# Kernel optimization log

Hardware: AMD Instinct MI355X
Metric: run time of the kernel (lower is better)

## Reference

```python
import jax, jax.numpy as jnp
import numpy as np

S = 30.0  # scale
M = 0.5   # angular margin

N, D, C = 1024, 512, 100000


def setup_inputs() -> dict:
    key = jax.random.key(0)
    k1, k2, k3 = jax.random.split(key, 3)
    embeddings = jax.random.normal(k1, (N, D), dtype=jnp.float32)
    weight = jax.random.normal(k2, (C, D), dtype=jnp.float32)
    labels = jax.random.randint(k3, (N,), 0, C, dtype=jnp.int64)
    return {"embeddings": embeddings, "weight": weight, "labels": labels}


def _l2norm(x, axis=-1, eps=1e-12):
    # matches torch F.normalize: x / max(||x||, eps)
    n = jnp.sqrt(jnp.sum(x * x, axis=axis, keepdims=True))
    return x / jnp.maximum(n, eps)


def reference(embeddings, weight, labels):
    e = _l2norm(embeddings)                      # [N, D]
    w = _l2norm(weight)                          # [C, D]
    cos_theta = jnp.clip(e @ w.T, -1.0, 1.0)     # [N, C]
    theta = jnp.arccos(cos_theta)
    cos_theta_m = jnp.cos(theta + M)
    # apply margin only at the label-indexed entry per row (one-hot blend)
    rows = jnp.arange(cos_theta.shape[0])
    target_vals = cos_theta_m[rows, labels]
    logits = cos_theta.at[rows, labels].set(target_vals)
    return S * logits
```

## Files before the change

### kernel.cpp

```cpp
#include <hip/hip_runtime.h>
#include <cstdint>
#include <cstddef>


constexpr int N_ROWS = 1024;
constexpr int DIM    = 512;
constexpr int C_CLS  = 100000;
constexpr int C_PAD  = 100096;

#define COS_M 0.87758256189037271612f
#define SIN_M 0.47942553860420300027f

typedef __attribute__((ext_vector_type(8))) __bf16 bf16x8;
typedef __attribute__((ext_vector_type(4))) float  floatx4;

__device__ inline unsigned short f2bf(float f) {
    unsigned int u = __float_as_uint(f);
    u += 0x7FFFu + ((u >> 16) & 1u);
    return (unsigned short)(u >> 16);
}

__device__ inline float wave_reduce_sum(float v) {
    v += __shfl_xor(v, 32, 64);
    v += __shfl_xor(v, 16, 64);
    v += __shfl_xor(v, 8, 64);
    v += __shfl_xor(v, 4, 64);
    v += __shfl_xor(v, 2, 64);
    v += __shfl_xor(v, 1, 64);
    return v;
}

__device__ inline void async16(const void* g, void* l) {
    __builtin_amdgcn_global_load_lds(
        (const __attribute__((address_space(1))) void*)g,
        (__attribute__((address_space(3))) void*)l,
        16, 0, 0);
}

__global__ __launch_bounds__(256) void normalize_rows(
    const float* __restrict__ in, unsigned short* __restrict__ out,
    int rows_valid, int rows_total) {
    int wave = (int)((blockIdx.x * 256u + threadIdx.x) >> 6);
    int lane = threadIdx.x & 63;
    if (wave >= rows_total) return;

    unsigned short* orow = out + (size_t)wave * DIM;
    if (wave < rows_valid) {
        const float4* rp = (const float4*)(in + (size_t)wave * DIM);
        float4 x0 = rp[lane];
        float4 x1 = rp[64 + lane];
        float s = x0.x*x0.x + x0.y*x0.y + x0.z*x0.z + x0.w*x0.w
                + x1.x*x1.x + x1.y*x1.y + x1.z*x1.z + x1.w*x1.w;
        s = wave_reduce_sum(s);
        float inv = 1.0f / fmaxf(sqrtf(s), 1e-12f);
        ushort4 o0, o1;
        o0.x = f2bf(x0.x * inv); o0.y = f2bf(x0.y * inv);
        o0.z = f2bf(x0.z * inv); o0.w = f2bf(x0.w * inv);
        o1.x = f2bf(x1.x * inv); o1.y = f2bf(x1.y * inv);
        o1.z = f2bf(x1.z * inv); o1.w = f2bf(x1.w * inv);
        ((ushort4*)orow)[lane]      = o0;
        ((ushort4*)orow)[64 + lane] = o1;
    } else {
        ushort4 z; z.x = z.y = z.z = z.w = 0;
        ((ushort4*)orow)[lane]      = z;
        ((ushort4*)orow)[64 + lane] = z;
    }
}

__global__ __launch_bounds__(256) void arcface_gemm(
    const unsigned short* __restrict__ A,
    const unsigned short* __restrict__ W,
    const int* __restrict__ labels,
    float* __restrict__ out) {
    __shared__ unsigned short As[128 * 32];
    __shared__ unsigned short Bs[128 * 32];
    __shared__ int labs[128];

    const int tid  = threadIdx.x;
    const int lane = tid & 63;
    const int wv   = tid >> 6;
    const int wr   = wv >> 1;
    const int wc   = wv & 1;
    const int mbase = blockIdx.x * 128;
    const int nbase = blockIdx.y * 128;

    if (tid < 128) labs[tid] = labels[mbase + tid];

    const int srow   = tid >> 2;
    const int schunk = tid & 3;

    floatx4 acc[4][4];
    for (int i = 0; i < 4; i++)
        for (int j = 0; j < 4; j++)
            acc[i][j] = (floatx4){0.f, 0.f, 0.f, 0.f};

    const unsigned short* Ag = A + (size_t)mbase * DIM;
    const unsigned short* Wg = W + (size_t)nbase * DIM;

    const int kq   = (lane >> 4) * 8;
    const int mrow = lane & 15;

    for (int k0 = 0; k0 < DIM; k0 += 32) {
        async16(Ag + (size_t)srow * DIM + k0 + schunk * 8,        &As[tid * 8]);
        async16(Ag + (size_t)(srow + 64) * DIM + k0 + schunk * 8, &As[2048 + tid * 8]);
        async16(Wg + (size_t)srow * DIM + k0 + schunk * 8,        &Bs[tid * 8]);
        async16(Wg + (size_t)(srow + 64) * DIM + k0 + schunk * 8, &Bs[2048 + tid * 8]);
        __syncthreads();

        bf16x8 af[4], bfr[4];
        for (int i = 0; i < 4; i++)
            af[i] = *(const bf16x8*)&As[(wr * 64 + i * 16 + mrow) * 32 + kq];
        for (int j = 0; j < 4; j++)
            bfr[j] = *(const bf16x8*)&Bs[(wc * 64 + j * 16 + mrow) * 32 + kq];

        for (int i = 0; i < 4; i++)
            for (int j = 0; j < 4; j++)
                acc[i][j] = __builtin_amdgcn_mfma_f32_16x16x32_bf16(
                    af[i], bfr[j], acc[i][j], 0, 0, 0);
        __syncthreads();
    }

    const int col0 = nbase + wc * 64 + (lane & 15);
    for (int i = 0; i < 4; i++) {
        const int rbase = wr * 64 + i * 16 + (lane >> 4) * 4;
        for (int r = 0; r < 4; r++) {
            const int row  = rbase + r;
            const int grow = mbase + row;
            const int lab  = labs[row];
            float* orow = out + (size_t)grow * C_CLS;
            for (int j = 0; j < 4; j++) {
                const int gc = col0 + j * 16;
                if (gc < C_CLS) {
                    float c = acc[i][j][r];
                    c = fminf(1.0f, fmaxf(-1.0f, c));
                    float v = c;
                    if (gc == lab) {
                        v = COS_M * c - SIN_M * sqrtf(fmaxf(0.0f, 1.0f - c * c));
                    }
                    orow[gc] = 30.0f * v;
                }
            }
        }
    }
}

extern "C" void kernel_launch(void* const* d_in, const int* in_sizes, int n_in,
                              void* d_out, int out_size, void* d_ws, size_t ws_size,
                              hipStream_t stream) {
    const float* emb    = (const float*)d_in[0];
    const float* wgt    = (const float*)d_in[1];
    const int*   labels = (const int*)d_in[2];
    float*       out    = (float*)d_out;

    unsigned short* An = (unsigned short*)d_ws;
    unsigned short* Wn = (unsigned short*)((char*)d_ws + (size_t)N_ROWS * DIM * 2);

    normalize_rows<<<N_ROWS / 4, 256, 0, stream>>>(emb, An, N_ROWS, N_ROWS);
    normalize_rows<<<C_PAD / 4, 256, 0, stream>>>(wgt, Wn, C_CLS, C_PAD);

    dim3 grid(N_ROWS / 128, C_PAD / 128);
    arcface_gemm<<<grid, 256, 0, stream>>>(An, Wn, labels, out);
}
```

Before: 727.7 us.

## Fuse weight normalization into GEMM and remap blocks for XCD L2 reuse

Drops the separate weight-normalization kernel: the GEMM now loads fp32 weight rows directly, converts them to bf16 in registers, accumulates per-row sums of squares, and scales the accumulators by the inverse norm in the epilogue. Blocks are remapped so all M tiles of a weight panel land on the same XCD for L2 sharing, and LDS tiles use XOR swizzling to reduce bank conflicts. This removes a full read/write pass over the weight matrix, at the cost of twice the B-tile load bytes per K step and extra conversion work in the main loop.

```diff
diff --git a/kernel.cpp b/kernel.cpp
--- a/kernel.cpp
+++ b/kernel.cpp
@@ -6,7 +6,8 @@
 constexpr int N_ROWS = 1024;
 constexpr int DIM    = 512;
 constexpr int C_CLS  = 100000;
-constexpr int C_PAD  = 100096;
+constexpr int NPANEL = 784;
+constexpr int MTILES = 8;
 
 #define COS_M 0.87758256189037271612f
 #define SIN_M 0.47942553860420300027f
@@ -38,100 +39,165 @@
 }
 
 __global__ __launch_bounds__(256) void normalize_rows(
-    const float* __restrict__ in, unsigned short* __restrict__ out,
-    int rows_valid, int rows_total) {
+    const float* __restrict__ in, unsigned short* __restrict__ out, int rows) {
     int wave = (int)((blockIdx.x * 256u + threadIdx.x) >> 6);
     int lane = threadIdx.x & 63;
-    if (wave >= rows_total) return;
-
+    if (wave >= rows) return;
+
+    const float4* rp = (const float4*)(in + (size_t)wave * DIM);
+    float4 x0 = rp[lane];
+    float4 x1 = rp[64 + lane];
+    float s = x0.x*x0.x + x0.y*x0.y + x0.z*x0.z + x0.w*x0.w
+            + x1.x*x1.x + x1.y*x1.y + x1.z*x1.z + x1.w*x1.w;
+    s = wave_reduce_sum(s);
+    float inv = 1.0f / fmaxf(sqrtf(s), 1e-12f);
     unsigned short* orow = out + (size_t)wave * DIM;
-    if (wave < rows_valid) {
-        const float4* rp = (const float4*)(in + (size_t)wave * DIM);
-        float4 x0 = rp[lane];
-        float4 x1 = rp[64 + lane];
-        float s = x0.x*x0.x + x0.y*x0.y + x0.z*x0.z + x0.w*x0.w
-                + x1.x*x1.x + x1.y*x1.y + x1.z*x1.z + x1.w*x1.w;
-        s = wave_reduce_sum(s);
-        float inv = 1.0f / fmaxf(sqrtf(s), 1e-12f);
-        ushort4 o0, o1;
-        o0.x = f2bf(x0.x * inv); o0.y = f2bf(x0.y * inv);
-        o0.z = f2bf(x0.z * inv); o0.w = f2bf(x0.w * inv);
-        o1.x = f2bf(x1.x * inv); o1.y = f2bf(x1.y * inv);
-        o1.z = f2bf(x1.z * inv); o1.w = f2bf(x1.w * inv);
-        ((ushort4*)orow)[lane]      = o0;
-        ((ushort4*)orow)[64 + lane] = o1;
-    } else {
-        ushort4 z; z.x = z.y = z.z = z.w = 0;
-        ((ushort4*)orow)[lane]      = z;
-        ((ushort4*)orow)[64 + lane] = z;
-    }
+    ushort4 o0, o1;
+    o0.x = f2bf(x0.x * inv); o0.y = f2bf(x0.y * inv);
+    o0.z = f2bf(x0.z * inv); o0.w = f2bf(x0.w * inv);
+    o1.x = f2bf(x1.x * inv); o1.y = f2bf(x1.y * inv);
+    o1.z = f2bf(x1.z * inv); o1.w = f2bf(x1.w * inv);
+    ((ushort4*)orow)[lane]      = o0;
+    ((ushort4*)orow)[64 + lane] = o1;
 }
 
 __global__ __launch_bounds__(256) void arcface_gemm(
     const unsigned short* __restrict__ A,
-    const unsigned short* __restrict__ W,
+    const float* __restrict__ Wf,
     const int* __restrict__ labels,
     float* __restrict__ out) {
     __shared__ unsigned short As[128 * 32];
-    __shared__ unsigned short Bs[128 * 32];
-    __shared__ int labs[128];
+    __shared__ float          Bs[128 * 32];
+    __shared__ int   labs[128];
+    __shared__ float winv[128];
 
     const int tid  = threadIdx.x;
     const int lane = tid & 63;
     const int wv   = tid >> 6;
     const int wr   = wv >> 1;
     const int wc   = wv & 1;
-    const int mbase = blockIdx.x * 128;
-    const int nbase = blockIdx.y * 128;
+
+    const int bid   = blockIdx.x;
+    const int xcd   = bid & 7;
+    const int s     = bid >> 3;
+    const int panel = xcd * (NPANEL / 8) + (s >> 3);
+    const int mtile = s & 7;
+    const int mbase = mtile * 128;
+    const int nbase = panel * 128;
 
     if (tid < 128) labs[tid] = labels[mbase + tid];
 
-    const int srow   = tid >> 2;
-    const int schunk = tid & 3;
+    const int arow0  = tid >> 2;
+    const int aslot0 = (tid & 3) ^ (arow0 & 3);
+    const int arow1  = arow0 + 64;
+    const int aslot1 = (tid & 3) ^ (arow1 & 3);
+    size_t bsrc[4];
+    #pragma unroll
+    for (int q = 0; q < 4; q++) {
+        int c    = tid + 256 * q;
+        int row  = c >> 3;
+        int slot = (c & 7) ^ (row & 7);
+        int grow = nbase + row;
+        if (grow > C_CLS - 1) grow = C_CLS - 1;
+        bsrc[q] = (size_t)grow * DIM + (size_t)(slot * 4);
+    }
+
+    const unsigned short* Ag = A + (size_t)mbase * DIM;
+
+    const int kq   = (lane >> 4) * 8;
+    const int mrow = lane & 15;
+
+    int aidx[4];
+    #pragma unroll
+    for (int i = 0; i < 4; i++) {
+        int row = wr * 64 + i * 16 + mrow;
+        aidx[i] = row * 32 + (((kq >> 3) ^ (row & 3)) << 3);
+    }
+    int bidx0[4], bidx1[4];
+    #pragma unroll
+    for (int j = 0; j < 4; j++) {
+        int row  = wc * 64 + j * 16 + mrow;
+        bidx0[j] = row * 32 + ((((kq >> 2)    ) ^ (row & 7)) << 2);
+        bidx1[j] = row * 32 + ((((kq >> 2) + 1) ^ (row & 7)) << 2);
+    }
 
     floatx4 acc[4][4];
+    #pragma unroll
     for (int i = 0; i < 4; i++)
+        #pragma unroll
         for (int j = 0; j < 4; j++)
             acc[i][j] = (floatx4){0.f, 0.f, 0.f, 0.f};
-
-    const unsigned short* Ag = A + (size_t)mbase * DIM;
-    const unsigned short* Wg = W + (size_t)nbase * DIM;
-
-    const int kq   = (lane >> 4) * 8;
-    const int mrow = lane & 15;
+    float ssq[2] = {0.f, 0.f};
 
     for (int k0 = 0; k0 < DIM; k0 += 32) {
-        async16(Ag + (size_t)srow * DIM + k0 + schunk * 8,        &As[tid * 8]);
-        async16(Ag + (size_t)(srow + 64) * DIM + k0 + schunk * 8, &As[2048 + tid * 8]);
-        async16(Wg + (size_t)srow * DIM + k0 + schunk * 8,        &Bs[tid * 8]);
-        async16(Wg + (size_t)(srow + 64) * DIM + k0 + schunk * 8, &Bs[2048 + tid * 8]);
+        async16(Ag + (size_t)arow0 * DIM + k0 + aslot0 * 8, &As[tid * 8]);
+        async16(Ag + (size_t)arow1 * DIM + k0 + aslot1 * 8, &As[2048 + tid * 8]);
+        #pragma unroll
+        for (int q = 0; q < 4; q++)
+            async16(Wf + bsrc[q] + k0, &Bs[(tid + 256 * q) * 4]);
         __syncthreads();
 
         bf16x8 af[4], bfr[4];
+        #pragma unroll
         for (int i = 0; i < 4; i++)
-            af[i] = *(const bf16x8*)&As[(wr * 64 + i * 16 + mrow) * 32 + kq];
-        for (int j = 0; j < 4; j++)
-            bfr[j] = *(const bf16x8*)&Bs[(wc * 64 + j * 16 + mrow) * 32 + kq];
-
+            af[i] = *(const bf16x8*)&As[aidx[i]];
+        #pragma unroll
+        for (int j = 0; j < 4; j++) {
+            float4 lo = *(const float4*)&Bs[bidx0[j]];
+            float4 hi = *(const float4*)&Bs[bidx1[j]];
+            bf16x8 b;
+            b[0] = (__bf16)lo.x; b[1] = (__bf16)lo.y;
+            b[2] = (__bf16)lo.z; b[3] = (__bf16)lo.w;
+            b[4] = (__bf16)hi.x; b[5] = (__bf16)hi.y;
+            b[6] = (__bf16)hi.z; b[7] = (__bf16)hi.w;
+            bfr[j] = b;
+            if (wr == (j >> 1)) {
+                float t = ssq[j & 1];
+                t = fmaf(lo.x, lo.x, t); t = fmaf(lo.y, lo.y, t);
+                t = fmaf(lo.z, lo.z, t); t = fmaf(lo.w, lo.w, t);
+                t = fmaf(hi.x, hi.x, t); t = fmaf(hi.y, hi.y, t);
+                t = fmaf(hi.z, hi.z, t); t = fmaf(hi.w, hi.w, t);
+                ssq[j & 1] = t;
+            }
+        }
+        #pragma unroll
         for (int i = 0; i < 4; i++)
+            #pragma unroll
             for (int j = 0; j < 4; j++)
                 acc[i][j] = __builtin_amdgcn_mfma_f32_16x16x32_bf16(
                     af[i], bfr[j], acc[i][j], 0, 0, 0);
         __syncthreads();
     }
 
-    const int col0 = nbase + wc * 64 + (lane & 15);
+    #pragma unroll
+    for (int jj = 0; jj < 2; jj++) {
+        float v = ssq[jj];
+        v += __shfl_xor(v, 16, 64);
+        v += __shfl_xor(v, 32, 64);
+        if (lane < 16)
+            winv[wc * 64 + wr * 32 + jj * 16 + lane] = 1.0f / fmaxf(sqrtf(v), 1e-12f);
+    }
+    __syncthreads();
+
+    float wnv[4];
+    #pragma unroll
+    for (int j = 0; j < 4; j++) wnv[j] = winv[wc * 64 + j * 16 + mrow];
+
+    const int col0 = nbase + wc * 64 + mrow;
+    #pragma unroll
     for (int i = 0; i < 4; i++) {
         const int rbase = wr * 64 + i * 16 + (lane >> 4) * 4;
+        #pragma unroll
         for (int r = 0; r < 4; r++) {
             const int row  = rbase + r;
             const int grow = mbase + row;
             const int lab  = labs[row];
             float* orow = out + (size_t)grow * C_CLS;
+            #pragma unroll
             for (int j = 0; j < 4; j++) {
                 const int gc = col0 + j * 16;
                 if (gc < C_CLS) {
-                    float c = acc[i][j][r];
+                    float c = acc[i][j][r] * wnv[j];
                     c = fminf(1.0f, fmaxf(-1.0f, c));
                     float v = c;
                     if (gc == lab) {
@@ -153,11 +219,7 @@
     float*       out    = (float*)d_out;
 
     unsigned short* An = (unsigned short*)d_ws;
-    unsigned short* Wn = (unsigned short*)((char*)d_ws + (size_t)N_ROWS * DIM * 2);
-
-    normalize_rows<<<N_ROWS / 4, 256, 0, stream>>>(emb, An, N_ROWS, N_ROWS);
-    normalize_rows<<<C_PAD / 4, 256, 0, stream>>>(wgt, Wn, C_CLS, C_PAD);
-
-    dim3 grid(N_ROWS / 128, C_PAD / 128);
-    arcface_gemm<<<grid, 256, 0, stream>>>(An, Wn, labels, out);
-}
+
+    normalize_rows<<<N_ROWS / 4, 256, 0, stream>>>(emb, An, N_ROWS);
+    arcface_gemm<<<dim3(MTILES * NPANEL), 256, 0, stream>>>(An, wgt, labels, out);
+}
```

Measured after the change: 737.6 us. About the same (+1.4%).

## Restructure ArcFace GEMM: direct global fragment loads, 128x256 tiles, XCD-aware panel mapping

Applied to the files above, without the earlier changes.

The GEMM kernel drops LDS staging and its per-k barriers, and each wave now loads its MFMA bf16 fragments straight from global memory with a fully unrolled k loop. Tiles grow to 128x256 with 512 threads per block, and a 1D grid is remapped so that the blocks on each XCD share the same weight panels, which should improve L2 reuse. Output writes become nontemporal stores, and the zero padding of weight rows is replaced by clamping the row index. The cost is uncoalesced, redundant global reads that now rely on the caches instead of shared memory, plus higher register pressure.

```diff
diff --git a/kernel.cpp b/kernel.cpp
--- a/kernel.cpp
+++ b/kernel.cpp
@@ -3,10 +3,11 @@
 #include <cstddef>
 
 
-constexpr int N_ROWS = 1024;
-constexpr int DIM    = 512;
-constexpr int C_CLS  = 100000;
-constexpr int C_PAD  = 100096;
+constexpr int N_ROWS  = 1024;
+constexpr int DIM     = 512;
+constexpr int C_CLS   = 100000;
+constexpr int NPANEL  = 392;
+constexpr int MTILES  = 8;
 
 #define COS_M 0.87758256189037271612f
 #define SIN_M 0.47942553860420300027f
@@ -30,104 +31,101 @@
     return v;
 }
 
-__device__ inline void async16(const void* g, void* l) {
-    __builtin_amdgcn_global_load_lds(
-        (const __attribute__((address_space(1))) void*)g,
-        (__attribute__((address_space(3))) void*)l,
-        16, 0, 0);
+__global__ __launch_bounds__(256) void normalize_rows(
+    const float* __restrict__ in, unsigned short* __restrict__ out, int rows) {
+    int wave = (int)((blockIdx.x * 256u + threadIdx.x) >> 6);
+    int lane = threadIdx.x & 63;
+    if (wave >= rows) return;
+
+    const float4* rp = (const float4*)(in + (size_t)wave * DIM);
+    float4 x0 = rp[lane];
+    float4 x1 = rp[64 + lane];
+    float s = x0.x*x0.x + x0.y*x0.y + x0.z*x0.z + x0.w*x0.w
+            + x1.x*x1.x + x1.y*x1.y + x1.z*x1.z + x1.w*x1.w;
+    s = wave_reduce_sum(s);
+    float inv = 1.0f / fmaxf(sqrtf(s), 1e-12f);
+    unsigned short* orow = out + (size_t)wave * DIM;
+    ushort4 o0, o1;
+    o0.x = f2bf(x0.x * inv); o0.y = f2bf(x0.y * inv);
+    o0.z = f2bf(x0.z * inv); o0.w = f2bf(x0.w * inv);
+    o1.x = f2bf(x1.x * inv); o1.y = f2bf(x1.y * inv);
+    o1.z = f2bf(x1.z * inv); o1.w = f2bf(x1.w * inv);
+    ((ushort4*)orow)[lane]      = o0;
+    ((ushort4*)orow)[64 + lane] = o1;
 }
 
-__global__ __launch_bounds__(256) void normalize_rows(
-    const float* __restrict__ in, unsigned short* __restrict__ out,
-    int rows_valid, int rows_total) {
-    int wave = (int)((blockIdx.x * 256u + threadIdx.x) >> 6);
-    int lane = threadIdx.x & 63;
-    if (wave >= rows_total) return;
-
-    unsigned short* orow = out + (size_t)wave * DIM;
-    if (wave < rows_valid) {
-        const float4* rp = (const float4*)(in + (size_t)wave * DIM);
-        float4 x0 = rp[lane];
-        float4 x1 = rp[64 + lane];
-        float s = x0.x*x0.x + x0.y*x0.y + x0.z*x0.z + x0.w*x0.w
-                + x1.x*x1.x + x1.y*x1.y + x1.z*x1.z + x1.w*x1.w;
-        s = wave_reduce_sum(s);
-        float inv = 1.0f / fmaxf(sqrtf(s), 1e-12f);
-        ushort4 o0, o1;
-        o0.x = f2bf(x0.x * inv); o0.y = f2bf(x0.y * inv);
-        o0.z = f2bf(x0.z * inv); o0.w = f2bf(x0.w * inv);
-        o1.x = f2bf(x1.x * inv); o1.y = f2bf(x1.y * inv);
-        o1.z = f2bf(x1.z * inv); o1.w = f2bf(x1.w * inv);
-        ((ushort4*)orow)[lane]      = o0;
-        ((ushort4*)orow)[64 + lane] = o1;
-    } else {
-        ushort4 z; z.x = z.y = z.z = z.w = 0;
-        ((ushort4*)orow)[lane]      = z;
-        ((ushort4*)orow)[64 + lane] = z;
-    }
-}
-
-__global__ __launch_bounds__(256) void arcface_gemm(
+__global__ __launch_bounds__(512, 2) void arcface_gemm(
     const unsigned short* __restrict__ A,
-    const unsigned short* __restrict__ W,
+    const unsigned short* __restrict__ Wn,
     const int* __restrict__ labels,
     float* __restrict__ out) {
-    __shared__ unsigned short As[128 * 32];
-    __shared__ unsigned short Bs[128 * 32];
     __shared__ int labs[128];
 
     const int tid  = threadIdx.x;
     const int lane = tid & 63;
     const int wv   = tid >> 6;
-    const int wr   = wv >> 1;
-    const int wc   = wv & 1;
-    const int mbase = blockIdx.x * 128;
-    const int nbase = blockIdx.y * 128;
+    const int wr   = wv >> 2;
+    const int wc   = wv & 3;
+    const int mrow = lane & 15;
+    const int kq8  = lane >> 4;
+
+    const int bid   = blockIdx.x;
+    const int xcd   = bid & 7;
+    const int s     = bid >> 3;
+    const int panel = xcd * (NPANEL / 8) + (s >> 3);
+    const int mtile = s & 7;
+    const int mbase = mtile * 128;
+    const int nbase = panel * 256;
 
     if (tid < 128) labs[tid] = labels[mbase + tid];
+    __syncthreads();
 
-    const int srow   = tid >> 2;
-    const int schunk = tid & 3;
+    const unsigned short* pa[4];
+    const unsigned short* pb[4];
+    #pragma unroll
+    for (int i = 0; i < 4; i++) {
+        int ra = mbase + wr * 64 + i * 16 + mrow;
+        pa[i] = A + (size_t)ra * DIM + kq8 * 8;
+        int rb = nbase + wc * 64 + i * 16 + mrow;
+        if (rb > C_CLS - 1) rb = C_CLS - 1;
+        pb[i] = Wn + (size_t)rb * DIM + kq8 * 8;
+    }
 
     floatx4 acc[4][4];
+    #pragma unroll
     for (int i = 0; i < 4; i++)
+        #pragma unroll
         for (int j = 0; j < 4; j++)
             acc[i][j] = (floatx4){0.f, 0.f, 0.f, 0.f};
 
-    const unsigned short* Ag = A + (size_t)mbase * DIM;
-    const unsigned short* Wg = W + (size_t)nbase * DIM;
-
-    const int kq   = (lane >> 4) * 8;
-    const int mrow = lane & 15;
-
-    for (int k0 = 0; k0 < DIM; k0 += 32) {
-        async16(Ag + (size_t)srow * DIM + k0 + schunk * 8,        &As[tid * 8]);
-        async16(Ag + (size_t)(srow + 64) * DIM + k0 + schunk * 8, &As[2048 + tid * 8]);
-        async16(Wg + (size_t)srow * DIM + k0 + schunk * 8,        &Bs[tid * 8]);
-        async16(Wg + (size_t)(srow + 64) * DIM + k0 + schunk * 8, &Bs[2048 + tid * 8]);
-        __syncthreads();
-
+    #pragma unroll
+    for (int ks = 0; ks < 16; ks++) {
         bf16x8 af[4], bfr[4];
+        #pragma unroll
         for (int i = 0; i < 4; i++)
-            af[i] = *(const bf16x8*)&As[(wr * 64 + i * 16 + mrow) * 32 + kq];
+            af[i] = *(const bf16x8*)(pa[i] + ks * 32);
+        #pragma unroll
         for (int j = 0; j < 4; j++)
-            bfr[j] = *(const bf16x8*)&Bs[(wc * 64 + j * 16 + mrow) * 32 + kq];
-
+            bfr[j] = *(const bf16x8*)(pb[j] + ks * 32);
+        #pragma unroll
         for (int i = 0; i < 4; i++)
+            #pragma unroll
             for (int j = 0; j < 4; j++)
                 acc[i][j] = __builtin_amdgcn_mfma_f32_16x16x32_bf16(
                     af[i], bfr[j], acc[i][j], 0, 0, 0);
-        __syncthreads();
     }
 
-    const int col0 = nbase + wc * 64 + (lane & 15);
+    const int col0 = nbase + wc * 64 + mrow;
+    #pragma unroll
     for (int i = 0; i < 4; i++) {
         const int rbase = wr * 64 + i * 16 + (lane >> 4) * 4;
+        #pragma unroll
         for (int r = 0; r < 4; r++) {
             const int row  = rbase + r;
             const int grow = mbase + row;
             const int lab  = labs[row];
             float* orow = out + (size_t)grow * C_CLS;
+            #pragma unroll
             for (int j = 0; j < 4; j++) {
                 const int gc = col0 + j * 16;
                 if (gc < C_CLS) {
@@ -137,7 +135,7 @@
                     if (gc == lab) {
                         v = COS_M * c - SIN_M * sqrtf(fmaxf(0.0f, 1.0f - c * c));
                     }
-                    orow[gc] = 30.0f * v;
+                    __builtin_nontemporal_store(30.0f * v, &orow[gc]);
                 }
             }
         }
@@ -155,9 +153,7 @@
     unsigned short* An = (unsigned short*)d_ws;
     unsigned short* Wn = (unsigned short*)((char*)d_ws + (size_t)N_ROWS * DIM * 2);
 
-    normalize_rows<<<N_ROWS / 4, 256, 0, stream>>>(emb, An, N_ROWS, N_ROWS);
-    normalize_rows<<<C_PAD / 4, 256, 0, stream>>>(wgt, Wn, C_CLS, C_PAD);
-
-    dim3 grid(N_ROWS / 128, C_PAD / 128);
-    arcface_gemm<<<grid, 256, 0, stream>>>(An, Wn, labels, out);
+    normalize_rows<<<N_ROWS / 4, 256, 0, stream>>>(emb, An, N_ROWS);
+    normalize_rows<<<C_CLS / 4, 256, 0, stream>>>(wgt, Wn, C_CLS);
+    arcface_gemm<<<dim3(MTILES * NPANEL), 512, 0, stream>>>(An, Wn, labels, out);
 }
```

Result: slower. 914.6 us (+25.7%).
